# Kernel tuning notes

Measured on AMD Instinct MI355X. Metric: run time of the kernel, lower is better.

The kernel has to match this reference:

```python
import jax, jax.numpy as jnp
import numpy as np

PS = 4          # patch size
C = 3           # channels
VOCAB = 512
D = 256         # embed dim
PD = PS * PS * C  # 48 patch dim


def _gelu(x):
    return jax.nn.gelu(x, approximate=False)  # torch nn.GELU default = exact erf


def setup_inputs() -> dict:
    key = jax.random.key(0)
    ks = jax.random.split(key, 16)
    frames = jax.random.uniform(ks[0], (32, 256, 256, 3), jnp.float32) * 255.0

    def lin(kw, kb, fan_in, fan_out):
        bound = 1.0 / np.sqrt(fan_in)
        w = jax.random.uniform(kw, (fan_out, fan_in), jnp.float32, -bound, bound)
        b = jax.random.uniform(kb, (fan_out,), jnp.float32, -bound, bound)
        return w, b

    enc_w1, enc_b1 = lin(ks[1], ks[2], PD, D)
    enc_w2, enc_b2 = lin(ks[3], ks[4], D, D)
    enc_w3, enc_b3 = lin(ks[5], ks[6], D, D)
    dec_w1, dec_b1 = lin(ks[7], ks[8], D, D)
    dec_w2, dec_b2 = lin(ks[9], ks[10], D, D)
    dec_w3, dec_b3 = lin(ks[11], ks[12], D, PD)
    codebook = jax.random.normal(ks[13], (VOCAB, D), jnp.float32) * 0.1
    return {
        'frames': frames,
        'enc_w1': enc_w1, 'enc_b1': enc_b1,
        'enc_w2': enc_w2, 'enc_b2': enc_b2,
        'enc_w3': enc_w3, 'enc_b3': enc_b3,
        'codebook': codebook,
        'dec_w1': dec_w1, 'dec_b1': dec_b1,
        'dec_w2': dec_w2, 'dec_b2': dec_b2,
        'dec_w3': dec_w3, 'dec_b3': dec_b3,
    }


def _patchify(x):  # [B,H,W,C] -> [B, N, ps*ps*C]
    B, H, W, Ch = x.shape
    h, w = H // PS, W // PS
    x = x.reshape(B, h, PS, w, PS, Ch).transpose(0, 1, 3, 2, 4, 5)
    return x.reshape(B, h * w, PS * PS * Ch)


def _unpatchify(p):  # [B, N, ps*ps*C] -> [B,H,W,C]
    B, N, _ = p.shape
    h = w = int(np.sqrt(N))
    p = p.reshape(B, h, w, PS, PS, C).transpose(0, 1, 3, 2, 4, 5)
    return p.reshape(B, h * PS, w * PS, C)


def reference(frames, enc_w1, enc_b1, enc_w2, enc_b2, enc_w3, enc_b3,
              codebook, dec_w1, dec_b1, dec_w2, dec_b2, dec_w3, dec_b3):
    x = frames / 255.0 * 2.0 - 1.0
    patches = _patchify(x)  # [B,N,48]
    # encoder MLP
    z = _gelu(patches @ enc_w1.T + enc_b1)
    z = _gelu(z @ enc_w2.T + enc_b2)
    z_e = z @ enc_w3.T + enc_b3  # [B,N,D]
    # nearest-codebook lookup (squared L2; argmin equals cdist argmin)
    d2 = (jnp.sum(z_e * z_e, -1, keepdims=True)
          - 2.0 * jnp.einsum('bnd,vd->bnv', z_e, codebook)
          + jnp.sum(codebook * codebook, -1))  # [B,N,V]
    tokens = jnp.argmin(d2, axis=-1)  # [B,N] int
    z_q = codebook[tokens]  # [B,N,D]
    z_q_st = z_e + jax.lax.stop_gradient(z_q - z_e)
    # decoder MLP
    y = _gelu(z_q_st @ dec_w1.T + dec_b1)
    y = _gelu(y @ dec_w2.T + dec_b2)
    y = y @ dec_w3.T + dec_b3  # [B,N,48]
    recon = _unpatchify(y)
    target = frames / 255.0 * 2.0 - 1.0
    recon_loss = jnp.mean((recon - target) ** 2)
    commitment_loss = jnp.mean((z_e - jax.lax.stop_gradient(z_q)) ** 2)
    codebook_loss = jnp.mean((z_q - jax.lax.stop_gradient(z_e)) ** 2)
    return recon, tokens, recon_loss, commitment_loss, codebook_loss
```

## Files before the change

### kernel.cpp

```cpp
#include <hip/hip_runtime.h>
#include <hip/hip_bf16.h>
#include <math.h>
#include <float.h>
#include <limits.h>

#define T_ROWS 131072

typedef __attribute__((ext_vector_type(8))) short short8;
typedef __attribute__((ext_vector_type(4))) float f32x4;

__device__ __forceinline__ float gelu_f(float x){
    return 0.5f * x * (1.0f + erff(x * 0.7071067811865475f));
}
__device__ __forceinline__ float bf2f(ushort u){
    union { unsigned int i; float f; } v; v.i = ((unsigned int)u) << 16; return v.f;
}
__device__ __forceinline__ ushort f2bf(float f){
    union { float f; unsigned int i; } v; v.f = f;
    unsigned int i = v.i;
    unsigned int r = (i + 0x7fffu + ((i >> 16) & 1u)) >> 16;
    return (ushort)r;
}
__device__ __forceinline__ void split3(float x, ushort &u0, ushort &u1, ushort &u2){
    union { float f; unsigned int i; } v; v.f = x;
    u0 = (ushort)(v.i >> 16);
    union { unsigned int i; float f; } h0; h0.i = ((unsigned int)u0) << 16;
    float r = x - h0.f;
    union { float f; unsigned int i; } vr; vr.f = r;
    u1 = (ushort)(vr.i >> 16);
    union { unsigned int i; float f; } h1; h1.i = ((unsigned int)u1) << 16;
    float r2 = r - h1.f;
    union { float f; unsigned int i; } v2; v2.f = r2;
    u2 = (ushort)(v2.i >> 16);
}

template<int K, bool GELU, int LOADER>
__global__ __launch_bounds__(256) void gemm_kernel(
    const float* __restrict__ Ain,
    const float* __restrict__ frames,
    const float* __restrict__ W,
    const float* __restrict__ bias,
    float* __restrict__ Cout)
{
    constexpr int BM=128, BN=128, BK=16;
    __shared__ __align__(16) float As[BK][BM+4];
    __shared__ __align__(16) float Ws[BK][BN+4];

    const int tid = threadIdx.x;
    const int tx = tid & 15, ty = tid >> 4;
    const int m0 = blockIdx.x * BM;
    const int c0 = blockIdx.y * BN;

    const int q  = tid & 3;
    const int r0 = tid >> 2;

    const float* aptr0 = nullptr;
    const float* aptr1 = nullptr;
    int base0 = 0, base1 = 0;
    if constexpr (LOADER == 0){
        aptr0 = Ain + (size_t)(m0 + r0) * K;
        aptr1 = aptr0 + (size_t)64 * K;
    } else {
        int p0 = m0 + r0;
        int b = p0 >> 12, nl = p0 & 4095, hh = nl >> 6, ww = nl & 63;
        base0 = ((b*256 + hh*4)*256 + ww*4)*3;
        int p1 = p0 + 64;
        b = p1 >> 12; nl = p1 & 4095; hh = nl >> 6; ww = nl & 63;
        base1 = ((b*256 + hh*4)*256 + ww*4)*3;
    }
    const float* wptr0 = W + (size_t)(c0 + r0) * K;
    const float* wptr1 = wptr0 + (size_t)64 * K;

    float acc[8][8];
    #pragma unroll
    for (int i=0;i<8;++i)
        #pragma unroll
        for (int j=0;j<8;++j) acc[i][j] = 0.0f;

    for (int k0 = 0; k0 < K; k0 += BK){
        const int k = k0 + q*4;
        float4 va, vb;
        if constexpr (LOADER == 1){
            const int ph = k / 12, rem = k - ph*12;
            va = *(const float4*)(frames + base0 + ph*768 + rem);
            vb = *(const float4*)(frames + base1 + ph*768 + rem);
            const float sc = 2.0f/255.0f;
            va.x = va.x*sc - 1.0f; va.y = va.y*sc - 1.0f;
            va.z = va.z*sc - 1.0f; va.w = va.w*sc - 1.0f;
            vb.x = vb.x*sc - 1.0f; vb.y = vb.y*sc - 1.0f;
            vb.z = vb.z*sc - 1.0f; vb.w = vb.w*sc - 1.0f;
        } else {
            va = *(const float4*)(aptr0 + k);
            vb = *(const float4*)(aptr1 + k);
        }
        As[q*4+0][r0]    = va.x; As[q*4+1][r0]    = va.y;
        As[q*4+2][r0]    = va.z; As[q*4+3][r0]    = va.w;
        As[q*4+0][r0+64] = vb.x; As[q*4+1][r0+64] = vb.y;
        As[q*4+2][r0+64] = vb.z; As[q*4+3][r0+64] = vb.w;

        float4 wa = *(const float4*)(wptr0 + k);
        float4 wb = *(const float4*)(wptr1 + k);
        Ws[q*4+0][r0]    = wa.x; Ws[q*4+1][r0]    = wa.y;
        Ws[q*4+2][r0]    = wa.z; Ws[q*4+3][r0]    = wa.w;
        Ws[q*4+0][r0+64] = wb.x; Ws[q*4+1][r0+64] = wb.y;
        Ws[q*4+2][r0+64] = wb.z; Ws[q*4+3][r0+64] = wb.w;

        __syncthreads();
        #pragma unroll
        for (int kk=0; kk<BK; ++kk){
            float a[8], b[8];
            *(float4*)&a[0] = *(const float4*)&As[kk][ty*4];
            *(float4*)&a[4] = *(const float4*)&As[kk][64+ty*4];
            *(float4*)&b[0] = *(const float4*)&Ws[kk][tx*4];
            *(float4*)&b[4] = *(const float4*)&Ws[kk][64+tx*4];
            #pragma unroll
            for (int i=0;i<8;++i)
                #pragma unroll
                for (int j=0;j<8;++j)
                    acc[i][j] = fmaf(a[i], b[j], acc[i][j]);
        }
        __syncthreads();
    }

    float bj[8];
    *(float4*)&bj[0] = *(const float4*)(bias + c0 + tx*4);
    *(float4*)&bj[4] = *(const float4*)(bias + c0 + 64 + tx*4);
    #pragma unroll
    for (int i=0;i<8;++i){
        const int row = m0 + ((i<4) ? (ty*4+i) : (64+ty*4+i-4));
        float o[8];
        #pragma unroll
        for (int j=0;j<8;++j){
            float x = acc[i][j] + bj[j];
            o[j] = GELU ? gelu_f(x) : x;
        }
        float* dst = Cout + (size_t)row*256 + c0 + tx*4;
        *(float4*)dst      = *(const float4*)&o[0];
        *(float4*)(dst+64) = *(const float4*)&o[4];
    }
}

__global__ __launch_bounds__(256) void wsplit_kernel(
    const float* __restrict__ w2, const float* __restrict__ w3,
    const float* __restrict__ d1, const float* __restrict__ d2,
    ushort* __restrict__ w2s0, ushort* __restrict__ w2s1, ushort* __restrict__ w2s2,
    ushort* __restrict__ w3s0, ushort* __restrict__ w3s1, ushort* __restrict__ w3s2,
    ushort* __restrict__ w1b, ushort* __restrict__ w2b)
{
    const int i = (blockIdx.x*256 + threadIdx.x)*4;
    float4 a = *(const float4*)(w2 + i);
    ushort4 s0, s1, s2;
    split3(a.x, s0.x, s1.x, s2.x); split3(a.y, s0.y, s1.y, s2.y);
    split3(a.z, s0.z, s1.z, s2.z); split3(a.w, s0.w, s1.w, s2.w);
    *(ushort4*)(w2s0+i)=s0; *(ushort4*)(w2s1+i)=s1; *(ushort4*)(w2s2+i)=s2;
    float4 b = *(const float4*)(w3 + i);
    split3(b.x, s0.x, s1.x, s2.x); split3(b.y, s0.y, s1.y, s2.y);
    split3(b.z, s0.z, s1.z, s2.z); split3(b.w, s0.w, s1.w, s2.w);
    *(ushort4*)(w3s0+i)=s0; *(ushort4*)(w3s1+i)=s1; *(ushort4*)(w3s2+i)=s2;
    float4 c = *(const float4*)(d1 + i);
    ushort4 u; u.x=f2bf(c.x); u.y=f2bf(c.y); u.z=f2bf(c.z); u.w=f2bf(c.w);
    *(ushort4*)(w1b+i) = u;
    float4 d = *(const float4*)(d2 + i);
    u.x=f2bf(d.x); u.y=f2bf(d.y); u.z=f2bf(d.z); u.w=f2bf(d.w);
    *(ushort4*)(w2b+i) = u;
}

__global__ __launch_bounds__(256) void cnorm_kernel(
    const float* __restrict__ cb, float* __restrict__ cn,
    ushort* __restrict__ cbb,
    ushort* __restrict__ cbs0, ushort* __restrict__ cbs1, ushort* __restrict__ cbs2)
{
    const int lane = threadIdx.x & 63;
    const int code = blockIdx.x*4 + (threadIdx.x >> 6);
    float4 v = ((const float4*)(cb + (size_t)code*256))[lane];
    size_t off = (size_t)code*256 + lane*4;
    ushort4 u; u.x=f2bf(v.x); u.y=f2bf(v.y); u.z=f2bf(v.z); u.w=f2bf(v.w);
    *(ushort4*)(cbb + off) = u;
    ushort4 s0, s1, s2;
    split3(v.x, s0.x, s1.x, s2.x); split3(v.y, s0.y, s1.y, s2.y);
    split3(v.z, s0.z, s1.z, s2.z); split3(v.w, s0.w, s1.w, s2.w);
    *(ushort4*)(cbs0 + off) = s0;
    *(ushort4*)(cbs1 + off) = s1;
    *(ushort4*)(cbs2 + off) = s2;
    float s = v.x*v.x + v.y*v.y + v.z*v.z + v.w*v.w;
    #pragma unroll
    for (int m=1; m<64; m<<=1) s += __shfl_xor(s, m);
    if (lane == 0) cn[code] = s;
}

template<bool GELU>
__global__ __launch_bounds__(256, 3) void split6_gemm(
    const float* __restrict__ Ain,
    const ushort* __restrict__ W0, const ushort* __restrict__ W1,
    const ushort* __restrict__ W2,
    const float* __restrict__ bias,
    float* __restrict__ Cout)
{
    __shared__ __align__(16) ushort Al[3][128][40];
    __shared__ __align__(16) ushort Wl[2][128][40];

    const int tid = threadIdx.x;
    const int m0 = blockIdx.x * 128;
    const int n0 = blockIdx.y * 128;
    const int srow = tid >> 1, shalf = (tid & 1) * 16;
    const int lane = tid & 63;
    const int w = tid >> 6;
    const int wm = (w >> 1) * 64, wn = (w & 1) * 64;
    const int lr = lane & 15, lg = lane >> 4;

    const float*  asrc = Ain + (size_t)(m0 + srow)*256 + shalf;
    const ushort* ws0  = W0  + (size_t)(n0 + srow)*256 + shalf;
    const ushort* ws1  = W1  + (size_t)(n0 + srow)*256 + shalf;
    const ushort* w2frag = W2 + (size_t)(n0 + wn + lr)*256 + lg*8;

    f32x4 acc[4][4];
    #pragma unroll
    for (int mi=0;mi<4;++mi)
        #pragma unroll
        for (int ni=0;ni<4;++ni)
            acc[mi][ni] = (f32x4){0.f,0.f,0.f,0.f};

    for (int k0=0; k0<256; k0+=32){
        float x[16];
        *(float4*)&x[0]  = *(const float4*)(asrc + k0);
        *(float4*)&x[4]  = *(const float4*)(asrc + k0 + 4);
        *(float4*)&x[8]  = *(const float4*)(asrc + k0 + 8);
        *(float4*)&x[12] = *(const float4*)(asrc + k0 + 12);
        ushort t0[16], t1[16], t2[16];
        #pragma unroll
        for (int e=0;e<16;++e) split3(x[e], t0[e], t1[e], t2[e]);
        *(uint4*)&Al[0][srow][shalf]   = *(const uint4*)&t0[0];
        *(uint4*)&Al[0][srow][shalf+8] = *(const uint4*)&t0[8];
        *(uint4*)&Al[1][srow][shalf]   = *(const uint4*)&t1[0];
        *(uint4*)&Al[1][srow][shalf+8] = *(const uint4*)&t1[8];
        *(uint4*)&Al[2][srow][shalf]   = *(const uint4*)&t2[0];
        *(uint4*)&Al[2][srow][shalf+8] = *(const uint4*)&t2[8];
        *(uint4*)&Wl[0][srow][shalf]   = *(const uint4*)(ws0 + k0);
        *(uint4*)&Wl[0][srow][shalf+8] = *(const uint4*)(ws0 + k0 + 8);
        *(uint4*)&Wl[1][srow][shalf]   = *(const uint4*)(ws1 + k0);
        *(uint4*)&Wl[1][srow][shalf+8] = *(const uint4*)(ws1 + k0 + 8);
        short8 b2[4];
        #pragma unroll
        for (int ni=0;ni<4;++ni)
            b2[ni] = *(const short8*)(w2frag + (size_t)ni*16*256 + k0);
        __syncthreads();

        short8 b0[4], b1[4];
        #pragma unroll
        for (int ni=0;ni<4;++ni){
            b0[ni] = *(const short8*)&Wl[0][wn + ni*16 + lr][lg*8];
            b1[ni] = *(const short8*)&Wl[1][wn + ni*16 + lr][lg*8];
        }
        #pragma unroll
        for (int mi=0;mi<4;++mi){
            short8 a0 = *(const short8*)&Al[0][wm + mi*16 + lr][lg*8];
            short8 a1 = *(const short8*)&Al[1][wm + mi*16 + lr][lg*8];
            short8 a2 = *(const short8*)&Al[2][wm + mi*16 + lr][lg*8];
            #pragma unroll
            for (int ni=0;ni<4;++ni)
                acc[mi][ni] = __builtin_amdgcn_mfma_f32_16x16x32_bf16(a0, b0[ni], acc[mi][ni], 0,0,0);
            #pragma unroll
            for (int ni=0;ni<4;++ni)
                acc[mi][ni] = __builtin_amdgcn_mfma_f32_16x16x32_bf16(a0, b1[ni], acc[mi][ni], 0,0,0);
            #pragma unroll
            for (int ni=0;ni<4;++ni)
                acc[mi][ni] = __builtin_amdgcn_mfma_f32_16x16x32_bf16(a1, b0[ni], acc[mi][ni], 0,0,0);
            #pragma unroll
            for (int ni=0;ni<4;++ni)
                acc[mi][ni] = __builtin_amdgcn_mfma_f32_16x16x32_bf16(a0, b2[ni], acc[mi][ni], 0,0,0);
            #pragma unroll
            for (int ni=0;ni<4;++ni)
                acc[mi][ni] = __builtin_amdgcn_mfma_f32_16x16x32_bf16(a1, b1[ni], acc[mi][ni], 0,0,0);
            #pragma unroll
            for (int ni=0;ni<4;++ni)
                acc[mi][ni] = __builtin_amdgcn_mfma_f32_16x16x32_bf16(a2, b0[ni], acc[mi][ni], 0,0,0);
        }
        __syncthreads();
    }

    float bn[4];
    #pragma unroll
    for (int ni=0;ni<4;++ni) bn[ni] = bias[n0 + wn + ni*16 + lr];
    #pragma unroll
    for (int mi=0;mi<4;++mi)
        #pragma unroll
        for (int ni=0;ni<4;++ni)
            #pragma unroll
            for (int r=0;r<4;++r){
                int row = m0 + wm + mi*16 + lg*4 + r;
                float v = acc[mi][ni][r] + bn[ni];
                if (GELU) v = gelu_f(v);
                Cout[(size_t)row*256 + n0 + wn + ni*16 + lr] = v;
            }
}

#define INSERT1(dv, iv) do { \
    float _d = (dv); int _i = (iv); \
    if (_d < bd || (_d == bd && _i < bi)){ bd = _d; bi = _i; } \
} while(0)

__global__ __launch_bounds__(256, 3) void tokens_split6(
    const float* __restrict__ Zf,
    const ushort* __restrict__ C0, const ushort* __restrict__ C1,
    const ushort* __restrict__ C2,
    const float* __restrict__ cn,
    float2* __restrict__ partials,
    float* __restrict__ zz_out)
{
    __shared__ __align__(16) ushort Al[3][128][40];
    __shared__ __align__(16) ushort Wl[2][128][40];
    __shared__ float2 ptop[128][2];

    const int tid = threadIdx.x;
    const int m0 = blockIdx.x * 128;
    const int n0 = blockIdx.y * 128;
    const int srow = tid >> 1, shalf = (tid & 1) * 16;
    const int lane = tid & 63;
    const int w = tid >> 6;
    const int wm = (w >> 1) * 64, wn = (w & 1) * 64;
    const int lr = lane & 15, lg = lane >> 4;

    const float*  asrc = Zf + (size_t)(m0 + srow)*256 + shalf;
    const ushort* ws0  = C0 + (size_t)(n0 + srow)*256 + shalf;
    const ushort* ws1  = C1 + (size_t)(n0 + srow)*256 + shalf;
    const ushort* c2frag = C2 + (size_t)(n0 + wn + lr)*256 + lg*8;

    f32x4 acc[4][4];
    #pragma unroll
    for (int mi=0;mi<4;++mi)
        #pragma unroll
        for (int ni=0;ni<4;++ni)
            acc[mi][ni] = (f32x4){0.f,0.f,0.f,0.f};

    float zzp = 0.0f;

    for (int k0=0; k0<256; k0+=32){
        float x[16];
        *(float4*)&x[0]  = *(const float4*)(asrc + k0);
        *(float4*)&x[4]  = *(const float4*)(asrc + k0 + 4);
        *(float4*)&x[8]  = *(const float4*)(asrc + k0 + 8);
        *(float4*)&x[12] = *(const float4*)(asrc + k0 + 12);
        ushort t0[16], t1[16], t2[16];
        #pragma unroll
        for (int e=0;e<16;++e){
            split3(x[e], t0[e], t1[e], t2[e]);
            zzp = fmaf(x[e], x[e], zzp);
        }
        *(uint4*)&Al[0][srow][shalf]   = *(const uint4*)&t0[0];
        *(uint4*)&Al[0][srow][shalf+8] = *(const uint4*)&t0[8];
        *(uint4*)&Al[1][srow][shalf]   = *(const uint4*)&t1[0];
        *(uint4*)&Al[1][srow][shalf+8] = *(const uint4*)&t1[8];
        *(uint4*)&Al[2][srow][shalf]   = *(const uint4*)&t2[0];
        *(uint4*)&Al[2][srow][shalf+8] = *(const uint4*)&t2[8];
        *(uint4*)&Wl[0][srow][shalf]   = *(const uint4*)(ws0 + k0);
        *(uint4*)&Wl[0][srow][shalf+8] = *(const uint4*)(ws0 + k0 + 8);
        *(uint4*)&Wl[1][srow][shalf]   = *(const uint4*)(ws1 + k0);
        *(uint4*)&Wl[1][srow][shalf+8] = *(const uint4*)(ws1 + k0 + 8);
        short8 b2[4];
        #pragma unroll
        for (int ni=0;ni<4;++ni)
            b2[ni] = *(const short8*)(c2frag + (size_t)ni*16*256 + k0);
        __syncthreads();

        short8 b0[4], b1[4];
        #pragma unroll
        for (int ni=0;ni<4;++ni){
            b0[ni] = *(const short8*)&Wl[0][wn + ni*16 + lr][lg*8];
            b1[ni] = *(const short8*)&Wl[1][wn + ni*16 + lr][lg*8];
        }
        #pragma unroll
        for (int mi=0;mi<4;++mi){
            short8 a0 = *(const short8*)&Al[0][wm + mi*16 + lr][lg*8];
            short8 a1 = *(const short8*)&Al[1][wm + mi*16 + lr][lg*8];
            short8 a2 = *(const short8*)&Al[2][wm + mi*16 + lr][lg*8];
            #pragma unroll
            for (int ni=0;ni<4;++ni)
                acc[mi][ni] = __builtin_amdgcn_mfma_f32_16x16x32_bf16(a0, b0[ni], acc[mi][ni], 0,0,0);
            #pragma unroll
            for (int ni=0;ni<4;++ni)
                acc[mi][ni] = __builtin_amdgcn_mfma_f32_16x16x32_bf16(a0, b1[ni], acc[mi][ni], 0,0,0);
            #pragma unroll
            for (int ni=0;ni<4;++ni)
                acc[mi][ni] = __builtin_amdgcn_mfma_f32_16x16x32_bf16(a1, b0[ni], acc[mi][ni], 0,0,0);
            #pragma unroll
            for (int ni=0;ni<4;++ni)
                acc[mi][ni] = __builtin_amdgcn_mfma_f32_16x16x32_bf16(a0, b2[ni], acc[mi][ni], 0,0,0);
            #pragma unroll
            for (int ni=0;ni<4;++ni)
                acc[mi][ni] = __builtin_amdgcn_mfma_f32_16x16x32_bf16(a1, b1[ni], acc[mi][ni], 0,0,0);
            #pragma unroll
            for (int ni=0;ni<4;++ni)
                acc[mi][ni] = __builtin_amdgcn_mfma_f32_16x16x32_bf16(a2, b0[ni], acc[mi][ni], 0,0,0);
        }
        __syncthreads();
    }

    {
        float other = __shfl_xor(zzp, 1);
        if (blockIdx.y == 0 && (tid & 1) == 0)
            zz_out[m0 + srow] = zzp + other;
    }

    float cnl[4];
    #pragma unroll
    for (int ni=0;ni<4;++ni) cnl[ni] = cn[n0 + wn + ni*16 + lr];

    #pragma unroll
    for (int mi=0;mi<4;++mi)
        #pragma unroll
        for (int r=0;r<4;++r){
            float bd = FLT_MAX; int bi = INT_MAX;
            #pragma unroll
            for (int ni=0;ni<4;++ni){
                float d = cnl[ni] - 2.0f*acc[mi][ni][r];
                int col = n0 + wn + ni*16 + lr;
                INSERT1(d, col);
            }
            #pragma unroll
            for (int m=1; m<16; m<<=1){
                float od = __shfl_xor(bd, m);
                int   oi = __shfl_xor(bi, m);
                INSERT1(od, oi);
            }
            if (lr == 0)
                ptop[wm + mi*16 + lg*4 + r][w & 1] = make_float2(bd, (float)bi);
        }
    __syncthreads();
    if (tid < 128){
        float2 hA = ptop[tid][0], hB = ptop[tid][1];
        int   gA = (int)hA.y, gB = (int)hB.y;
        bool takeB = (hB.x < hA.x) || (hB.x == hA.x && gB < gA);
        partials[(size_t)(m0 + tid)*4 + blockIdx.y] = takeB ? hB : hA;
    }
}

__global__ __launch_bounds__(256) void token_reduce(
    const float* __restrict__ zz_out, const float2* __restrict__ partials,
    float* __restrict__ tokf, float* __restrict__ loss)
{
    const int tid = threadIdx.x;
    const int row = blockIdx.x*256 + tid;
    float2 p0 = partials[(size_t)row*4 + 0];
    float2 p1 = partials[(size_t)row*4 + 1];
    float2 p2 = partials[(size_t)row*4 + 2];
    float2 p3 = partials[(size_t)row*4 + 3];
    float d = p0.x; int g = (int)p0.y;
    if (p1.x < d || (p1.x == d && (int)p1.y < g)){ d = p1.x; g = (int)p1.y; }
    if (p2.x < d || (p2.x == d && (int)p2.y < g)){ d = p2.x; g = (int)p2.y; }
    if (p3.x < d || (p3.x == d && (int)p3.y < g)){ d = p3.x; g = (int)p3.y; }
    tokf[row] = (float)g;
    float cs = zz_out[row] + d;
    #pragma unroll
    for (int m=1; m<64; m<<=1) cs += __shfl_xor(cs, m);
    __shared__ float wsum[4];
    const int lane = tid & 63, w = tid >> 6;
    if (lane == 0) wsum[w] = cs;
    __syncthreads();
    if (tid == 0) atomicAdd(loss + 1, wsum[0]+wsum[1]+wsum[2]+wsum[3]);
}

template<int LOADER>
__global__ __launch_bounds__(256) void mfma_gemm(
    const ushort* __restrict__ Abf,
    const ushort* __restrict__ cbb,
    const float* __restrict__ tokf,
    const ushort* __restrict__ Wbf,
    const float* __restrict__ bias,
    ushort* __restrict__ Ybf)
{
    __shared__ __align__(16) ushort Al[128][40];
    __shared__ __align__(16) ushort Wl[128][40];

    const int tid = threadIdx.x;
    const int m0 = blockIdx.x * 128;
    const int n0 = blockIdx.y * 128;
    const int srow = tid >> 1, shalf = (tid & 1) * 16;
    const int lane = tid & 63;
    const int w = tid >> 6;
    const int wm = (w >> 1) * 64, wn = (w & 1) * 64;
    const int lr = lane & 15, lg = lane >> 4;

    const ushort* asrc;
    if constexpr (LOADER == 1){
        int g = (int)tokf[m0 + srow];
        asrc = cbb + (size_t)g*256 + shalf;
    } else {
        asrc = Abf + (size_t)(m0 + srow)*256 + shalf;
    }
    const ushort* wsrc = Wbf + (size_t)(n0 + srow)*256 + shalf;

    f32x4 acc[4][4];
    #pragma unroll
    for (int mi=0;mi<4;++mi)
        #pragma unroll
        for (int ni=0;ni<4;++ni)
            acc[mi][ni] = (f32x4){0.f,0.f,0.f,0.f};

    for (int k0=0; k0<256; k0+=32){
        *(uint4*)&Al[srow][shalf]   = *(const uint4*)(asrc + k0);
        *(uint4*)&Al[srow][shalf+8] = *(const uint4*)(asrc + k0 + 8);
        *(uint4*)&Wl[srow][shalf]   = *(const uint4*)(wsrc + k0);
        *(uint4*)&Wl[srow][shalf+8] = *(const uint4*)(wsrc + k0 + 8);
// ... 127 lines not shown

__global__ void finalize_kernel(float* __restrict__ loss){
    if (threadIdx.x == 0 && blockIdx.x == 0){
        loss[0] = loss[0] * (1.0f/6291456.0f);
        float c = loss[1] * (1.0f/33554432.0f);
        loss[1] = c;
        loss[2] = c;
    }
}

extern "C" void kernel_launch(void* const* d_in, const int* in_sizes, int n_in,
                              void* d_out, int out_size, void* d_ws, size_t ws_size,
                              hipStream_t stream)
{
    (void)in_sizes; (void)n_in; (void)out_size; (void)ws_size;
    const float* frames   = (const float*)d_in[0];
    const float* enc_w1   = (const float*)d_in[1];
    const float* enc_b1   = (const float*)d_in[2];
    const float* enc_w2   = (const float*)d_in[3];
    const float* enc_b2   = (const float*)d_in[4];
    const float* enc_w3   = (const float*)d_in[5];
    const float* enc_b3   = (const float*)d_in[6];
    const float* codebook = (const float*)d_in[7];
    const float* dec_w1   = (const float*)d_in[8];
    const float* dec_b1   = (const float*)d_in[9];
    const float* dec_w2   = (const float*)d_in[10];
    const float* dec_b2   = (const float*)d_in[11];
    const float* dec_w3   = (const float*)d_in[12];
    const float* dec_b3   = (const float*)d_in[13];

    float* P = (float*)d_ws;
    float* Q = P + (size_t)33554432;
    float2* partials = (float2*)(Q + 18000000);
    ushort* Y1 = (ushort*)P;
    ushort* Y2 = (ushort*)Q;

    float* recon = (float*)d_out;
    float* tokf  = recon + 6291456;
    float* loss  = tokf + 131072;
    float*  cn   = recon;
    ushort* cbb  = (ushort*)(recon + 512);
    ushort* w1b  = (ushort*)(recon + 66048);
    ushort* w2b  = (ushort*)(recon + 98816);
    ushort* w2s0 = (ushort*)(recon + 131584);
    ushort* w2s1 = (ushort*)(recon + 164352);
    ushort* w2s2 = (ushort*)(recon + 197120);
    ushort* w3s0 = (ushort*)(recon + 229888);
    ushort* w3s1 = (ushort*)(recon + 262656);
    ushort* w3s2 = (ushort*)(recon + 295424);
    ushort* cbs0 = (ushort*)(recon + 328192);
    ushort* cbs1 = (ushort*)(recon + 393728);
    ushort* cbs2 = (ushort*)(recon + 459264);
    float*  zzb  = recon + 524800;

    hipMemsetAsync(loss, 0, 3*sizeof(float), stream);

    dim3 blk(256), grid2(T_ROWS/128, 2);
    wsplit_kernel<<<dim3(64), blk, 0, stream>>>(enc_w2, enc_w3, dec_w1, dec_w2,
        w2s0, w2s1, w2s2, w3s0, w3s1, w3s2, w1b, w2b);
    cnorm_kernel<<<dim3(128), blk, 0, stream>>>(codebook, cn, cbb, cbs0, cbs1, cbs2);
    gemm_kernel<48, true, 1><<<grid2, blk, 0, stream>>>(nullptr, frames, enc_w1, enc_b1, P);
    split6_gemm<true ><<<grid2, blk, 0, stream>>>(P, w2s0, w2s1, w2s2, enc_b2, Q);
    split6_gemm<false><<<grid2, blk, 0, stream>>>(Q, w3s0, w3s1, w3s2, enc_b3, P);
    tokens_split6<<<dim3(T_ROWS/128, 4), blk, 0, stream>>>(P, cbs0, cbs1, cbs2, cn, partials, zzb);
    token_reduce<<<dim3(T_ROWS/256), blk, 0, stream>>>(zzb, partials, tokf, loss);
    mfma_gemm<1><<<grid2, blk, 0, stream>>>(nullptr, cbb, tokf, w1b, dec_b1, Y1);
    mfma_gemm<0><<<grid2, blk, 0, stream>>>(Y1, nullptr, nullptr, w2b, dec_b2, Y2);
    dec3_mfma<<<dim3(T_ROWS/256), blk, 0, stream>>>(Y2, dec_w3, dec_b3, frames, recon, loss);
    finalize_kernel<<<dim3(1), dim3(64), 0, stream>>>(loss);
}
```

Before: 727.0 us.

## Retile split-bf16 GEMMs to full-width N, move enc layer 1 to MFMA, merge prep kernels

The weight-split and codebook-norm kernels become one prep kernel, which also pads and splits enc_w1 and folds the input normalization into a modified bias. The first encoder layer moves from the scalar FP32 GEMM to the split-bf16 MFMA kernel, reading raw frames and applying the 2/255 scale in the epilogue. The split6 and token kernels now use 64-row tiles spanning all 256 output columns (or half the codebook), so each activation row is loaded and split once instead of per N tile. The cost is more LDS for the weight tile, direct global loads for two of the three weight fragments, and a smaller row tile.

```diff
diff --git a/kernel.cpp b/kernel.cpp
--- a/kernel.cpp
+++ b/kernel.cpp
@@ -34,184 +34,104 @@
     u2 = (ushort)(v2.i >> 16);
 }
 
-template<int K, bool GELU, int LOADER>
-__global__ __launch_bounds__(256) void gemm_kernel(
+__global__ __launch_bounds__(256) void prep_kernel(
+    const float* __restrict__ w2, const float* __restrict__ w3,
+    const float* __restrict__ d1, const float* __restrict__ d2,
+    const float* __restrict__ w1, const float* __restrict__ b1,
+    const float* __restrict__ cb,
+    ushort* __restrict__ w2s0, ushort* __restrict__ w2s1, ushort* __restrict__ w2s2,
+    ushort* __restrict__ w3s0, ushort* __restrict__ w3s1, ushort* __restrict__ w3s2,
+    ushort* __restrict__ w1b, ushort* __restrict__ w2b,
+    float* __restrict__ cn, ushort* __restrict__ cbb,
+    ushort* __restrict__ cbs0, ushort* __restrict__ cbs1, ushort* __restrict__ cbs2,
+    ushort* __restrict__ w1p0, ushort* __restrict__ w1p1, ushort* __restrict__ w1p2,
+    float* __restrict__ bias2)
+{
+    const int blk = blockIdx.x, tid = threadIdx.x;
+    if (blk < 64){
+        const int i = (blk*256 + tid)*4;
+        float4 a = *(const float4*)(w2 + i);
+        ushort4 s0, s1, s2;
+        split3(a.x, s0.x, s1.x, s2.x); split3(a.y, s0.y, s1.y, s2.y);
+        split3(a.z, s0.z, s1.z, s2.z); split3(a.w, s0.w, s1.w, s2.w);
+        *(ushort4*)(w2s0+i)=s0; *(ushort4*)(w2s1+i)=s1; *(ushort4*)(w2s2+i)=s2;
+        float4 b = *(const float4*)(w3 + i);
+        split3(b.x, s0.x, s1.x, s2.x); split3(b.y, s0.y, s1.y, s2.y);
+        split3(b.z, s0.z, s1.z, s2.z); split3(b.w, s0.w, s1.w, s2.w);
+        *(ushort4*)(w3s0+i)=s0; *(ushort4*)(w3s1+i)=s1; *(ushort4*)(w3s2+i)=s2;
+        float4 c = *(const float4*)(d1 + i);
+        ushort4 u; u.x=f2bf(c.x); u.y=f2bf(c.y); u.z=f2bf(c.z); u.w=f2bf(c.w);
+        *(ushort4*)(w1b+i) = u;
+        float4 d = *(const float4*)(d2 + i);
+        u.x=f2bf(d.x); u.y=f2bf(d.y); u.z=f2bf(d.z); u.w=f2bf(d.w);
+        *(ushort4*)(w2b+i) = u;
+    } else if (blk < 192){
+        const int lane = tid & 63;
+        const int code = (blk-64)*4 + (tid >> 6);
+        float4 v = ((const float4*)(cb + (size_t)code*256))[lane];
+        size_t off = (size_t)code*256 + lane*4;
+        ushort4 u; u.x=f2bf(v.x); u.y=f2bf(v.y); u.z=f2bf(v.z); u.w=f2bf(v.w);
+        *(ushort4*)(cbb + off) = u;
+        ushort4 s0, s1, s2;
+        split3(v.x, s0.x, s1.x, s2.x); split3(v.y, s0.y, s1.y, s2.y);
+        split3(v.z, s0.z, s1.z, s2.z); split3(v.w, s0.w, s1.w, s2.w);
+        *(ushort4*)(cbs0 + off) = s0;
+        *(ushort4*)(cbs1 + off) = s1;
+        *(ushort4*)(cbs2 + off) = s2;
+        float s = v.x*v.x + v.y*v.y + v.z*v.z + v.w*v.w;
+        #pragma unroll
+        for (int m=1; m<64; m<<=1) s += __shfl_xor(s, m);
+        if (lane == 0) cn[code] = s;
+    } else if (blk < 208){
+        const int idx = (blk-192)*256 + tid;
+        const int n = idx >> 4, k = (idx & 15)*4;
+        ushort4 s0 = {0,0,0,0}, s1 = {0,0,0,0}, s2 = {0,0,0,0};
+        if (k < 48){
+            float4 v = *(const float4*)(w1 + n*48 + k);
+            split3(v.x, s0.x, s1.x, s2.x); split3(v.y, s0.y, s1.y, s2.y);
+            split3(v.z, s0.z, s1.z, s2.z); split3(v.w, s0.w, s1.w, s2.w);
+        }
+        *(ushort4*)(w1p0 + n*64 + k) = s0;
+        *(ushort4*)(w1p1 + n*64 + k) = s1;
+        *(ushort4*)(w1p2 + n*64 + k) = s2;
+    } else {
+        float s = 0.0f;
+        for (int k=0;k<48;++k) s += w1[tid*48 + k];
+        bias2[tid] = b1[tid] - s;
+    }
+}
+
+template<int KTOT, bool GELU, int LOADER, bool SCALE>
+__global__ __launch_bounds__(256, 3) void split6_gemm(
     const float* __restrict__ Ain,
     const float* __restrict__ frames,
-    const float* __restrict__ W,
-    const float* __restrict__ bias,
-    float* __restrict__ Cout)
-{
-    constexpr int BM=128, BN=128, BK=16;
-    __shared__ __align__(16) float As[BK][BM+4];
-    __shared__ __align__(16) float Ws[BK][BN+4];
-
-    const int tid = threadIdx.x;
-    const int tx = tid & 15, ty = tid >> 4;
-    const int m0 = blockIdx.x * BM;
-    const int c0 = blockIdx.y * BN;
-
-    const int q  = tid & 3;
-    const int r0 = tid >> 2;
-
-    const float* aptr0 = nullptr;
-    const float* aptr1 = nullptr;
-    int base0 = 0, base1 = 0;
-    if constexpr (LOADER == 0){
-        aptr0 = Ain + (size_t)(m0 + r0) * K;
-        aptr1 = aptr0 + (size_t)64 * K;
-    } else {
-        int p0 = m0 + r0;
-        int b = p0 >> 12, nl = p0 & 4095, hh = nl >> 6, ww = nl & 63;
-        base0 = ((b*256 + hh*4)*256 + ww*4)*3;
-        int p1 = p0 + 64;
-        b = p1 >> 12; nl = p1 & 4095; hh = nl >> 6; ww = nl & 63;
-        base1 = ((b*256 + hh*4)*256 + ww*4)*3;
-    }
-    const float* wptr0 = W + (size_t)(c0 + r0) * K;
-    const float* wptr1 = wptr0 + (size_t)64 * K;
-
-    float acc[8][8];
-    #pragma unroll
-    for (int i=0;i<8;++i)
-        #pragma unroll
-        for (int j=0;j<8;++j) acc[i][j] = 0.0f;
-
-    for (int k0 = 0; k0 < K; k0 += BK){
-        const int k = k0 + q*4;
-        float4 va, vb;
-        if constexpr (LOADER == 1){
-            const int ph = k / 12, rem = k - ph*12;
-            va = *(const float4*)(frames + base0 + ph*768 + rem);
-            vb = *(const float4*)(frames + base1 + ph*768 + rem);
-            const float sc = 2.0f/255.0f;
-            va.x = va.x*sc - 1.0f; va.y = va.y*sc - 1.0f;
-            va.z = va.z*sc - 1.0f; va.w = va.w*sc - 1.0f;
-            vb.x = vb.x*sc - 1.0f; vb.y = vb.y*sc - 1.0f;
-            vb.z = vb.z*sc - 1.0f; vb.w = vb.w*sc - 1.0f;
-        } else {
-            va = *(const float4*)(aptr0 + k);
-            vb = *(const float4*)(aptr1 + k);
-        }
-        As[q*4+0][r0]    = va.x; As[q*4+1][r0]    = va.y;
-        As[q*4+2][r0]    = va.z; As[q*4+3][r0]    = va.w;
-        As[q*4+0][r0+64] = vb.x; As[q*4+1][r0+64] = vb.y;
-        As[q*4+2][r0+64] = vb.z; As[q*4+3][r0+64] = vb.w;
-
-        float4 wa = *(const float4*)(wptr0 + k);
-        float4 wb = *(const float4*)(wptr1 + k);
-        Ws[q*4+0][r0]    = wa.x; Ws[q*4+1][r0]    = wa.y;
-        Ws[q*4+2][r0]    = wa.z; Ws[q*4+3][r0]    = wa.w;
-        Ws[q*4+0][r0+64] = wb.x; Ws[q*4+1][r0+64] = wb.y;
-        Ws[q*4+2][r0+64] = wb.z; Ws[q*4+3][r0+64] = wb.w;
-
-        __syncthreads();
-        #pragma unroll
-        for (int kk=0; kk<BK; ++kk){
-            float a[8], b[8];
-            *(float4*)&a[0] = *(const float4*)&As[kk][ty*4];
-            *(float4*)&a[4] = *(const float4*)&As[kk][64+ty*4];
-            *(float4*)&b[0] = *(const float4*)&Ws[kk][tx*4];
-            *(float4*)&b[4] = *(const float4*)&Ws[kk][64+tx*4];
-            #pragma unroll
-            for (int i=0;i<8;++i)
-                #pragma unroll
-                for (int j=0;j<8;++j)
-                    acc[i][j] = fmaf(a[i], b[j], acc[i][j]);
-        }
-        __syncthreads();
-    }
-
-    float bj[8];
-    *(float4*)&bj[0] = *(const float4*)(bias + c0 + tx*4);
-    *(float4*)&bj[4] = *(const float4*)(bias + c0 + 64 + tx*4);
-    #pragma unroll
-    for (int i=0;i<8;++i){
-        const int row = m0 + ((i<4) ? (ty*4+i) : (64+ty*4+i-4));
-        float o[8];
-        #pragma unroll
-        for (int j=0;j<8;++j){
-            float x = acc[i][j] + bj[j];
-            o[j] = GELU ? gelu_f(x) : x;
-        }
-        float* dst = Cout + (size_t)row*256 + c0 + tx*4;
-        *(float4*)dst      = *(const float4*)&o[0];
-        *(float4*)(dst+64) = *(const float4*)&o[4];
-    }
-}
-
-__global__ __launch_bounds__(256) void wsplit_kernel(
-    const float* __restrict__ w2, const float* __restrict__ w3,
-    const float* __restrict__ d1, const float* __restrict__ d2,
-    ushort* __restrict__ w2s0, ushort* __restrict__ w2s1, ushort* __restrict__ w2s2,
-    ushort* __restrict__ w3s0, ushort* __restrict__ w3s1, ushort* __restrict__ w3s2,
-    ushort* __restrict__ w1b, ushort* __restrict__ w2b)
-{
-    const int i = (blockIdx.x*256 + threadIdx.x)*4;
-    float4 a = *(const float4*)(w2 + i);
-    ushort4 s0, s1, s2;
-    split3(a.x, s0.x, s1.x, s2.x); split3(a.y, s0.y, s1.y, s2.y);
-    split3(a.z, s0.z, s1.z, s2.z); split3(a.w, s0.w, s1.w, s2.w);
-    *(ushort4*)(w2s0+i)=s0; *(ushort4*)(w2s1+i)=s1; *(ushort4*)(w2s2+i)=s2;
-    float4 b = *(const float4*)(w3 + i);
-    split3(b.x, s0.x, s1.x, s2.x); split3(b.y, s0.y, s1.y, s2.y);
-    split3(b.z, s0.z, s1.z, s2.z); split3(b.w, s0.w, s1.w, s2.w);
-    *(ushort4*)(w3s0+i)=s0; *(ushort4*)(w3s1+i)=s1; *(ushort4*)(w3s2+i)=s2;
-    float4 c = *(const float4*)(d1 + i);
-    ushort4 u; u.x=f2bf(c.x); u.y=f2bf(c.y); u.z=f2bf(c.z); u.w=f2bf(c.w);
-    *(ushort4*)(w1b+i) = u;
-    float4 d = *(const float4*)(d2 + i);
-    u.x=f2bf(d.x); u.y=f2bf(d.y); u.z=f2bf(d.z); u.w=f2bf(d.w);
-    *(ushort4*)(w2b+i) = u;
-}
-
-__global__ __launch_bounds__(256) void cnorm_kernel(
-    const float* __restrict__ cb, float* __restrict__ cn,
-    ushort* __restrict__ cbb,
-    ushort* __restrict__ cbs0, ushort* __restrict__ cbs1, ushort* __restrict__ cbs2)
-{
-    const int lane = threadIdx.x & 63;
-    const int code = blockIdx.x*4 + (threadIdx.x >> 6);
-    float4 v = ((const float4*)(cb + (size_t)code*256))[lane];
-    size_t off = (size_t)code*256 + lane*4;
-    ushort4 u; u.x=f2bf(v.x); u.y=f2bf(v.y); u.z=f2bf(v.z); u.w=f2bf(v.w);
-    *(ushort4*)(cbb + off) = u;
-    ushort4 s0, s1, s2;
-    split3(v.x, s0.x, s1.x, s2.x); split3(v.y, s0.y, s1.y, s2.y);
-    split3(v.z, s0.z, s1.z, s2.z); split3(v.w, s0.w, s1.w, s2.w);
-    *(ushort4*)(cbs0 + off) = s0;
-    *(ushort4*)(cbs1 + off) = s1;
-    *(ushort4*)(cbs2 + off) = s2;
-    float s = v.x*v.x + v.y*v.y + v.z*v.z + v.w*v.w;
-    #pragma unroll
-    for (int m=1; m<64; m<<=1) s += __shfl_xor(s, m);
-    if (lane == 0) cn[code] = s;
-}
-
-template<bool GELU>
-__global__ __launch_bounds__(256, 3) void split6_gemm(
-    const float* __restrict__ Ain,
     const ushort* __restrict__ W0, const ushort* __restrict__ W1,
     const ushort* __restrict__ W2,
     const float* __restrict__ bias,
     float* __restrict__ Cout)
 {
-    __shared__ __align__(16) ushort Al[3][128][40];
-    __shared__ __align__(16) ushort Wl[2][128][40];
+    __shared__ __align__(16) ushort Al[3][64][40];
+    __shared__ __align__(16) ushort Wl[256][40];
 
     const int tid = threadIdx.x;
-    const int m0 = blockIdx.x * 128;
-    const int n0 = blockIdx.y * 128;
-    const int srow = tid >> 1, shalf = (tid & 1) * 16;
+    const int m0 = blockIdx.x * 64;
+    const int arow = tid >> 2, q = tid & 3;
     const int lane = tid & 63;
     const int w = tid >> 6;
-    const int wm = (w >> 1) * 64, wn = (w & 1) * 64;
     const int lr = lane & 15, lg = lane >> 4;
 
-    const float*  asrc = Ain + (size_t)(m0 + srow)*256 + shalf;
-    const ushort* ws0  = W0  + (size_t)(n0 + srow)*256 + shalf;
-    const ushort* ws1  = W1  + (size_t)(n0 + srow)*256 + shalf;
-    const ushort* w2frag = W2 + (size_t)(n0 + wn + lr)*256 + lg*8;
+    const float* asrc = nullptr;
+    int pbase = 0;
+    if constexpr (LOADER == 0){
+        asrc = Ain + (size_t)(m0 + arow)*KTOT + q*8;
+    } else {
+        int p = m0 + arow;
+        int b = p >> 12, nl = p & 4095, hh = nl >> 6, ww = nl & 63;
+        pbase = ((b*256 + hh*4)*256 + ww*4)*3;
+    }
+    const ushort* wsrc  = W0 + (size_t)tid*KTOT;
+    const ushort* w1frag = W1 + (size_t)(w*64 + lr)*KTOT + lg*8;
+    const ushort* w2frag = W2 + (size_t)(w*64 + lr)*KTOT + lg*8;
 
     f32x4 acc[4][4];
     #pragma unroll
@@ -220,77 +140,88 @@
         for (int ni=0;ni<4;++ni)
             acc[mi][ni] = (f32x4){0.f,0.f,0.f,0.f};
 
-    for (int k0=0; k0<256; k0+=32){
-        float x[16];
-        *(float4*)&x[0]  = *(const float4*)(asrc + k0);
-        *(float4*)&x[4]  = *(const float4*)(asrc + k0 + 4);
-        *(float4*)&x[8]  = *(const float4*)(asrc + k0 + 8);
-        *(float4*)&x[12] = *(const float4*)(asrc + k0 + 12);
-        ushort t0[16], t1[16], t2[16];
-        #pragma unroll
-        for (int e=0;e<16;++e) split3(x[e], t0[e], t1[e], t2[e]);
-        *(uint4*)&Al[0][srow][shalf]   = *(const uint4*)&t0[0];
-        *(uint4*)&Al[0][srow][shalf+8] = *(const uint4*)&t0[8];
-        *(uint4*)&Al[1][srow][shalf]   = *(const uint4*)&t1[0];
-        *(uint4*)&Al[1][srow][shalf+8] = *(const uint4*)&t1[8];
-        *(uint4*)&Al[2][srow][shalf]   = *(const uint4*)&t2[0];
-        *(uint4*)&Al[2][srow][shalf+8] = *(const uint4*)&t2[8];
-        *(uint4*)&Wl[0][srow][shalf]   = *(const uint4*)(ws0 + k0);
-        *(uint4*)&Wl[0][srow][shalf+8] = *(const uint4*)(ws0 + k0 + 8);
-        *(uint4*)&Wl[1][srow][shalf]   = *(const uint4*)(ws1 + k0);
-        *(uint4*)&Wl[1][srow][shalf+8] = *(const uint4*)(ws1 + k0 + 8);
-        short8 b2[4];
-        #pragma unroll
-        for (int ni=0;ni<4;++ni)
-            b2[ni] = *(const short8*)(w2frag + (size_t)ni*16*256 + k0);
-        __syncthreads();
-
-        short8 b0[4], b1[4];
+    for (int k0=0; k0<KTOT; k0+=32){
+        float x[8];
+        if constexpr (LOADER == 0){
+            *(float4*)&x[0] = *(const float4*)(asrc + k0);
+            *(float4*)&x[4] = *(const float4*)(asrc + k0 + 4);
+        } else {
+            #pragma unroll
+            for (int j=0;j<2;++j){
+                int kk = k0 + q*8 + j*4;
+                float4 v = {0.f,0.f,0.f,0.f};
+                if (kk < 48){
+                    int ph = kk/12, rem = kk - ph*12;
+                    v = *(const float4*)(frames + pbase + ph*768 + rem);
+                }
+                x[j*4+0]=v.x; x[j*4+1]=v.y; x[j*4+2]=v.z; x[j*4+3]=v.w;
+            }
+        }
+        ushort t0[8], t1[8], t2[8];
+        #pragma unroll
+        for (int e=0;e<8;++e) split3(x[e], t0[e], t1[e], t2[e]);
+        *(uint4*)&Al[0][arow][q*8] = *(const uint4*)t0;
+        *(uint4*)&Al[1][arow][q*8] = *(const uint4*)t1;
+        *(uint4*)&Al[2][arow][q*8] = *(const uint4*)t2;
+        *(uint4*)&Wl[tid][0]  = *(const uint4*)(wsrc + k0);
+        *(uint4*)&Wl[tid][8]  = *(const uint4*)(wsrc + k0 + 8);
+        *(uint4*)&Wl[tid][16] = *(const uint4*)(wsrc + k0 + 16);
+        *(uint4*)&Wl[tid][24] = *(const uint4*)(wsrc + k0 + 24);
+        short8 b1v[4], b2v[4];
         #pragma unroll
         for (int ni=0;ni<4;++ni){
-            b0[ni] = *(const short8*)&Wl[0][wn + ni*16 + lr][lg*8];
-            b1[ni] = *(const short8*)&Wl[1][wn + ni*16 + lr][lg*8];
-        }
+            b1v[ni] = *(const short8*)(w1frag + (size_t)ni*16*KTOT + k0);
+            b2v[ni] = *(const short8*)(w2frag + (size_t)ni*16*KTOT + k0);
+        }
+        __syncthreads();
+
+        short8 b0v[4];
+        #pragma unroll
+        for (int ni=0;ni<4;++ni)
+            b0v[ni] = *(const short8*)&Wl[w*64 + ni*16 + lr][lg*8];
         #pragma unroll
         for (int mi=0;mi<4;++mi){
-            short8 a0 = *(const short8*)&Al[0][wm + mi*16 + lr][lg*8];
-            short8 a1 = *(const short8*)&Al[1][wm + mi*16 + lr][lg*8];
-            short8 a2 = *(const short8*)&Al[2][wm + mi*16 + lr][lg*8];
-            #pragma unroll
-            for (int ni=0;ni<4;++ni)
-                acc[mi][ni] = __builtin_amdgcn_mfma_f32_16x16x32_bf16(a0, b0[ni], acc[mi][ni], 0,0,0);
-            #pragma unroll
-            for (int ni=0;ni<4;++ni)
-                acc[mi][ni] = __builtin_amdgcn_mfma_f32_16x16x32_bf16(a0, b1[ni], acc[mi][ni], 0,0,0);
-            #pragma unroll
-            for (int ni=0;ni<4;++ni)
-                acc[mi][ni] = __builtin_amdgcn_mfma_f32_16x16x32_bf16(a1, b0[ni], acc[mi][ni], 0,0,0);
-            #pragma unroll
-            for (int ni=0;ni<4;++ni)
-                acc[mi][ni] = __builtin_amdgcn_mfma_f32_16x16x32_bf16(a0, b2[ni], acc[mi][ni], 0,0,0);
-            #pragma unroll
-            for (int ni=0;ni<4;++ni)
-                acc[mi][ni] = __builtin_amdgcn_mfma_f32_16x16x32_bf16(a1, b1[ni], acc[mi][ni], 0,0,0);
-            #pragma unroll
-            for (int ni=0;ni<4;++ni)
-                acc[mi][ni] = __builtin_amdgcn_mfma_f32_16x16x32_bf16(a2, b0[ni], acc[mi][ni], 0,0,0);
-        }
-        __syncthreads();
-    }
-
+            short8 a0 = *(const short8*)&Al[0][mi*16 + lr][lg*8];
+            short8 a1 = *(const short8*)&Al[1][mi*16 + lr][lg*8];
+            short8 a2 = *(const short8*)&Al[2][mi*16 + lr][lg*8];
+            #pragma unroll
+            for (int ni=0;ni<4;++ni)
+                acc[mi][ni] = __builtin_amdgcn_mfma_f32_16x16x32_bf16(a0, b0v[ni], acc[mi][ni], 0,0,0);
+            #pragma unroll
+            for (int ni=0;ni<4;++ni)
+                acc[mi][ni] = __builtin_amdgcn_mfma_f32_16x16x32_bf16(a0, b1v[ni], acc[mi][ni], 0,0,0);
+            #pragma unroll
+            for (int ni=0;ni<4;++ni)
+                acc[mi][ni] = __builtin_amdgcn_mfma_f32_16x16x32_bf16(a1, b0v[ni], acc[mi][ni], 0,0,0);
+            #pragma unroll
+            for (int ni=0;ni<4;++ni)
+                acc[mi][ni] = __builtin_amdgcn_mfma_f32_16x16x32_bf16(a0, b2v[ni], acc[mi][ni], 0,0,0);
+            #pragma unroll
+            for (int ni=0;ni<4;++ni)
+                acc[mi][ni] = __builtin_amdgcn_mfma_f32_16x16x32_bf16(a1, b1v[ni], acc[mi][ni], 0,0,0);
+            #pragma unroll
+            for (int ni=0;ni<4;++ni)
+                acc[mi][ni] = __builtin_amdgcn_mfma_f32_16x16x32_bf16(a2, b0v[ni], acc[mi][ni], 0,0,0);
+        }
+        __syncthreads();
+    }
+
+    const float alpha = 2.0f/255.0f;
     float bn[4];
     #pragma unroll
-    for (int ni=0;ni<4;++ni) bn[ni] = bias[n0 + wn + ni*16 + lr];
+    for (int ni=0;ni<4;++ni) bn[ni] = bias[w*64 + ni*16 + lr];
     #pragma unroll
     for (int mi=0;mi<4;++mi)
         #pragma unroll
         for (int ni=0;ni<4;++ni)
             #pragma unroll
             for (int r=0;r<4;++r){
-                int row = m0 + wm + mi*16 + lg*4 + r;
-                float v = acc[mi][ni][r] + bn[ni];
+                int row = m0 + mi*16 + lg*4 + r;
+                float v;
+                if (SCALE) v = fmaf(alpha, acc[mi][ni][r], bn[ni]);
+                else       v = acc[mi][ni][r] + bn[ni];
                 if (GELU) v = gelu_f(v);
-                Cout[(size_t)row*256 + n0 + wn + ni*16 + lr] = v;
+                Cout[(size_t)row*256 + w*64 + ni*16 + lr] = v;
             }
 }
 
@@ -307,23 +238,23 @@
     float2* __restrict__ partials,
     float* __restrict__ zz_out)
 {
-    __shared__ __align__(16) ushort Al[3][128][40];
-    __shared__ __align__(16) ushort Wl[2][128][40];
-    __shared__ float2 ptop[128][2];
+    __shared__ __align__(16) ushort Al[3][64][40];
+    __shared__ __align__(16) ushort Wl[256][40];
+    __shared__ float2 ptop[64][4];
 
     const int tid = threadIdx.x;
-    const int m0 = blockIdx.x * 128;
-    const int n0 = blockIdx.y * 128;
-    const int srow = tid >> 1, shalf = (tid & 1) * 16;
+    const int m0 = blockIdx.x * 64;
+    const int cbk = blockIdx.y;
+    const int n0 = cbk * 256;
+    const int arow = tid >> 2, q = tid & 3;
     const int lane = tid & 63;
     const int w = tid >> 6;
-    const int wm = (w >> 1) * 64, wn = (w & 1) * 64;
     const int lr = lane & 15, lg = lane >> 4;
 
-    const float*  asrc = Zf + (size_t)(m0 + srow)*256 + shalf;
-    const ushort* ws0  = C0 + (size_t)(n0 + srow)*256 + shalf;
-    const ushort* ws1  = C1 + (size_t)(n0 + srow)*256 + shalf;
-    const ushort* c2frag = C2 + (size_t)(n0 + wn + lr)*256 + lg*8;
+    const float*  asrc = Zf + (size_t)(m0 + arow)*256 + q*8;
+    const ushort* wsrc = C0 + (size_t)(n0 + tid)*256;
+    const ushort* c1frag = C1 + (size_t)(n0 + w*64 + lr)*256 + lg*8;
+    const ushort* c2frag = C2 + (size_t)(n0 + w*64 + lr)*256 + lg*8;
 
     f32x4 acc[4][4];
     #pragma unroll
@@ -335,75 +266,70 @@
     float zzp = 0.0f;
 
     for (int k0=0; k0<256; k0+=32){
-        float x[16];
-        *(float4*)&x[0]  = *(const float4*)(asrc + k0);
-        *(float4*)&x[4]  = *(const float4*)(asrc + k0 + 4);
-        *(float4*)&x[8]  = *(const float4*)(asrc + k0 + 8);
-        *(float4*)&x[12] = *(const float4*)(asrc + k0 + 12);
-        ushort t0[16], t1[16], t2[16];
-        #pragma unroll
-        for (int e=0;e<16;++e){
+        float x[8];
+        *(float4*)&x[0] = *(const float4*)(asrc + k0);
+        *(float4*)&x[4] = *(const float4*)(asrc + k0 + 4);
+        ushort t0[8], t1[8], t2[8];
+        #pragma unroll
+        for (int e=0;e<8;++e){
             split3(x[e], t0[e], t1[e], t2[e]);
             zzp = fmaf(x[e], x[e], zzp);
         }
-        *(uint4*)&Al[0][srow][shalf]   = *(const uint4*)&t0[0];
-        *(uint4*)&Al[0][srow][shalf+8] = *(const uint4*)&t0[8];
-        *(uint4*)&Al[1][srow][shalf]   = *(const uint4*)&t1[0];
-        *(uint4*)&Al[1][srow][shalf+8] = *(const uint4*)&t1[8];
-        *(uint4*)&Al[2][srow][shalf]   = *(const uint4*)&t2[0];
-        *(uint4*)&Al[2][srow][shalf+8] = *(const uint4*)&t2[8];
-        *(uint4*)&Wl[0][srow][shalf]   = *(const uint4*)(ws0 + k0);
-        *(uint4*)&Wl[0][srow][shalf+8] = *(const uint4*)(ws0 + k0 + 8);
-        *(uint4*)&Wl[1][srow][shalf]   = *(const uint4*)(ws1 + k0);
-        *(uint4*)&Wl[1][srow][shalf+8] = *(const uint4*)(ws1 + k0 + 8);
-        short8 b2[4];
-        #pragma unroll
-        for (int ni=0;ni<4;++ni)
-            b2[ni] = *(const short8*)(c2frag + (size_t)ni*16*256 + k0);
-        __syncthreads();
-
-        short8 b0[4], b1[4];
+        *(uint4*)&Al[0][arow][q*8] = *(const uint4*)t0;
+        *(uint4*)&Al[1][arow][q*8] = *(const uint4*)t1;
+        *(uint4*)&Al[2][arow][q*8] = *(const uint4*)t2;
+        *(uint4*)&Wl[tid][0]  = *(const uint4*)(wsrc + k0);
+        *(uint4*)&Wl[tid][8]  = *(const uint4*)(wsrc + k0 + 8);
+        *(uint4*)&Wl[tid][16] = *(const uint4*)(wsrc + k0 + 16);
+        *(uint4*)&Wl[tid][24] = *(const uint4*)(wsrc + k0 + 24);
+        short8 b1v[4], b2v[4];
         #pragma unroll
         for (int ni=0;ni<4;++ni){
-            b0[ni] = *(const short8*)&Wl[0][wn + ni*16 + lr][lg*8];
-            b1[ni] = *(const short8*)&Wl[1][wn + ni*16 + lr][lg*8];
-        }
+            b1v[ni] = *(const short8*)(c1frag + (size_t)ni*16*256 + k0);
+            b2v[ni] = *(const short8*)(c2frag + (size_t)ni*16*256 + k0);
+        }
+        __syncthreads();
+
+        short8 b0v[4];
+        #pragma unroll
+        for (int ni=0;ni<4;++ni)
+            b0v[ni] = *(const short8*)&Wl[w*64 + ni*16 + lr][lg*8];
         #pragma unroll
         for (int mi=0;mi<4;++mi){
-            short8 a0 = *(const short8*)&Al[0][wm + mi*16 + lr][lg*8];
-            short8 a1 = *(const short8*)&Al[1][wm + mi*16 + lr][lg*8];
-            short8 a2 = *(const short8*)&Al[2][wm + mi*16 + lr][lg*8];
-            #pragma unroll
-            for (int ni=0;ni<4;++ni)
-                acc[mi][ni] = __builtin_amdgcn_mfma_f32_16x16x32_bf16(a0, b0[ni], acc[mi][ni], 0,0,0);
-            #pragma unroll
-            for (int ni=0;ni<4;++ni)
-                acc[mi][ni] = __builtin_amdgcn_mfma_f32_16x16x32_bf16(a0, b1[ni], acc[mi][ni], 0,0,0);
-            #pragma unroll
-            for (int ni=0;ni<4;++ni)
-                acc[mi][ni] = __builtin_amdgcn_mfma_f32_16x16x32_bf16(a1, b0[ni], acc[mi][ni], 0,0,0);
-            #pragma unroll
-            for (int ni=0;ni<4;++ni)
-                acc[mi][ni] = __builtin_amdgcn_mfma_f32_16x16x32_bf16(a0, b2[ni], acc[mi][ni], 0,0,0);
-            #pragma unroll
-            for (int ni=0;ni<4;++ni)
-                acc[mi][ni] = __builtin_amdgcn_mfma_f32_16x16x32_bf16(a1, b1[ni], acc[mi][ni], 0,0,0);
-            #pragma unroll
-            for (int ni=0;ni<4;++ni)
-                acc[mi][ni] = __builtin_amdgcn_mfma_f32_16x16x32_bf16(a2, b0[ni], acc[mi][ni], 0,0,0);
+            short8 a0 = *(const short8*)&Al[0][mi*16 + lr][lg*8];
+            short8 a1 = *(const short8*)&Al[1][mi*16 + lr][lg*8];
+            short8 a2 = *(const short8*)&Al[2][mi*16 + lr][lg*8];
+            #pragma unroll
+            for (int ni=0;ni<4;++ni)
+                acc[mi][ni] = __builtin_amdgcn_mfma_f32_16x16x32_bf16(a0, b0v[ni], acc[mi][ni], 0,0,0);
+            #pragma unroll
+            for (int ni=0;ni<4;++ni)
+                acc[mi][ni] = __builtin_amdgcn_mfma_f32_16x16x32_bf16(a0, b1v[ni], acc[mi][ni], 0,0,0);
+            #pragma unroll
+            for (int ni=0;ni<4;++ni)
+                acc[mi][ni] = __builtin_amdgcn_mfma_f32_16x16x32_bf16(a1, b0v[ni], acc[mi][ni], 0,0,0);
+            #pragma unroll
+            for (int ni=0;ni<4;++ni)
+                acc[mi][ni] = __builtin_amdgcn_mfma_f32_16x16x32_bf16(a0, b2v[ni], acc[mi][ni], 0,0,0);
+            #pragma unroll
+            for (int ni=0;ni<4;++ni)
+                acc[mi][ni] = __builtin_amdgcn_mfma_f32_16x16x32_bf16(a1, b1v[ni], acc[mi][ni], 0,0,0);
+            #pragma unroll
+            for (int ni=0;ni<4;++ni)
+                acc[mi][ni] = __builtin_amdgcn_mfma_f32_16x16x32_bf16(a2, b0v[ni], acc[mi][ni], 0,0,0);
         }
         __syncthreads();
     }
 
     {
-        float other = __shfl_xor(zzp, 1);
-        if (blockIdx.y == 0 && (tid & 1) == 0)
-            zz_out[m0 + srow] = zzp + other;
+        float s = zzp + __shfl_xor(zzp, 1);
+        s += __shfl_xor(s, 2);
+        if (cbk == 0 && q == 0) zz_out[m0 + arow] = s;
     }
 
     float cnl[4];
     #pragma unroll
-    for (int ni=0;ni<4;++ni) cnl[ni] = cn[n0 + wn + ni*16 + lr];
+    for (int ni=0;ni<4;++ni) cnl[ni] = cn[n0 + w*64 + ni*16 + lr];
 
     #pragma unroll
     for (int mi=0;mi<4;++mi)
@@ -413,7 +339,7 @@
             #pragma unroll
             for (int ni=0;ni<4;++ni){
                 float d = cnl[ni] - 2.0f*acc[mi][ni][r];
-                int col = n0 + wn + ni*16 + lr;
+                int col = n0 + w*64 + ni*16 + lr;
                 INSERT1(d, col);
             }
             #pragma unroll
@@ -423,14 +349,17 @@
                 INSERT1(od, oi);
             }
             if (lr == 0)
-                ptop[wm + mi*16 + lg*4 + r][w & 1] = make_float2(bd, (float)bi);
+                ptop[mi*16 + lg*4 + r][w] = make_float2(bd, (float)bi);
         }
     __syncthreads();
-    if (tid < 128){
-        float2 hA = ptop[tid][0], hB = ptop[tid][1];
-        int   gA = (int)hA.y, gB = (int)hB.y;
-        bool takeB = (hB.x < hA.x) || (hB.x == hA.x && gB < gA);
-        partials[(size_t)(m0 + tid)*4 + blockIdx.y] = takeB ? hB : hA;
+    if (tid < 64){
+        float2 h = ptop[tid][0];
+        #pragma unroll
+        for (int ww=1; ww<4; ++ww){
+            float2 o = ptop[tid][ww];
+            if (o.x < h.x) h = o;
+        }
+        partials[(size_t)(m0 + tid)*2 + cbk] = h;
     }
 }
 
@@ -440,14 +369,10 @@
 {
     const int tid = threadIdx.x;
     const int row = blockIdx.x*256 + tid;
-    float2 p0 = partials[(size_t)row*4 + 0];
-    float2 p1 = partials[(size_t)row*4 + 1];
-    float2 p2 = partials[(size_t)row*4 + 2];
-    float2 p3 = partials[(size_t)row*4 + 3];
+    float2 p0 = partials[(size_t)row*2 + 0];
+    float2 p1 = partials[(size_t)row*2 + 1];
     float d = p0.x; int g = (int)p0.y;
     if (p1.x < d || (p1.x == d && (int)p1.y < g)){ d = p1.x; g = (int)p1.y; }
-    if (p2.x < d || (p2.x == d && (int)p2.y < g)){ d = p2.x; g = (int)p2.y; }
-    if (p3.x < d || (p3.x == d && (int)p3.y < g)){ d = p3.x; g = (int)p3.y; }
     tokf[row] = (float)g;
     float cs = zz_out[row] + d;
     #pragma unroll
@@ -681,20 +606,25 @@
     ushort* cbs1 = (ushort*)(recon + 393728);
     ushort* cbs2 = (ushort*)(recon + 459264);
     float*  zzb  = recon + 524800;
+    ushort* w1p0 = (ushort*)(recon + 655872);
+    ushort* w1p1 = (ushort*)(recon + 664064);
+    ushort* w1p2 = (ushort*)(recon + 672256);
+    float*  bias2 = recon + 680448;
 
     hipMemsetAsync(loss, 0, 3*sizeof(float), stream);
 
-    dim3 blk(256), grid2(T_ROWS/128, 2);
-    wsplit_kernel<<<dim3(64), blk, 0, stream>>>(enc_w2, enc_w3, dec_w1, dec_w2,
-        w2s0, w2s1, w2s2, w3s0, w3s1, w3s2, w1b, w2b);
-    cnorm_kernel<<<dim3(128), blk, 0, stream>>>(codebook, cn, cbb, cbs0, cbs1, cbs2);
-    gemm_kernel<48, true, 1><<<grid2, blk, 0, stream>>>(nullptr, frames, enc_w1, enc_b1, P);
-    split6_gemm<true ><<<grid2, blk, 0, stream>>>(P, w2s0, w2s1, w2s2, enc_b2, Q);
-    split6_gemm<false><<<grid2, blk, 0, stream>>>(Q, w3s0, w3s1, w3s2, enc_b3, P);
-    tokens_split6<<<dim3(T_ROWS/128, 4), blk, 0, stream>>>(P, cbs0, cbs1, cbs2, cn, partials, zzb);
+    dim3 blk(256);
+    prep_kernel<<<dim3(209), blk, 0, stream>>>(enc_w2, enc_w3, dec_w1, dec_w2,
+        enc_w1, enc_b1, codebook,
+        w2s0, w2s1, w2s2, w3s0, w3s1, w3s2, w1b, w2b,
+        cn, cbb, cbs0, cbs1, cbs2, w1p0, w1p1, w1p2, bias2);
+    split6_gemm<64,  true, 1, true ><<<dim3(T_ROWS/64), blk, 0, stream>>>(nullptr, frames, w1p0, w1p1, w1p2, bias2, P);
+    split6_gemm<256, true, 0, false><<<dim3(T_ROWS/64), blk, 0, stream>>>(P, nullptr, w2s0, w2s1, w2s2, enc_b2, Q);
+    split6_gemm<256, false,0, false><<<dim3(T_ROWS/64), blk, 0, stream>>>(Q, nullptr, w3s0, w3s1, w3s2, enc_b3, P);
+    tokens_split6<<<dim3(T_ROWS/64, 2), blk, 0, stream>>>(P, cbs0, cbs1, cbs2, cn, partials, zzb);
     token_reduce<<<dim3(T_ROWS/256), blk, 0, stream>>>(zzb, partials, tokf, loss);
-    mfma_gemm<1><<<grid2, blk, 0, stream>>>(nullptr, cbb, tokf, w1b, dec_b1, Y1);
-    mfma_gemm<0><<<grid2, blk, 0, stream>>>(Y1, nullptr, nullptr, w2b, dec_b2, Y2);
+    mfma_gemm<1><<<dim3(T_ROWS/128, 2), blk, 0, stream>>>(nullptr, cbb, tokf, w1b, dec_b1, Y1);
+    mfma_gemm<0><<<dim3(T_ROWS/128, 2), blk, 0, stream>>>(Y1, nullptr, nullptr, w2b, dec_b2, Y2);
     dec3_mfma<<<dim3(T_ROWS/256), blk, 0, stream>>>(Y2, dec_w3, dec_b3, frames, recon, loss);
     finalize_kernel<<<dim3(1), dim3(64), 0, stream>>>(loss);
 }
```

Result: faster. 708.6 us (-2.5%).
